# Kernel optimization log

Measured on AMD Instinct MI355X. Metric: run time of the kernel, lower is better.

## Reference

```python
import jax, jax.numpy as jnp
import numpy as np

DECAY_CONSTANT = 1.0


def _build_decay_matrices(weight, decay_value, S, dtype):
    """Build the row-repeat and col-repeat upper-triangular decay matrices.

    Wr[i, j] = w0[i] * (clip(dv0,0.9,1) ** (j-i) / C)   for j >= i, else 0
    Wc[i, j] = w1[j] *  clip(dv1,0.9,1) ** ((j-i) / C)  for j >= i, else 0
    """
    i = jnp.arange(S)[:, None]
    j = jnp.arange(S)[None, :]
    mask = j >= i
    # Clamp exponent to 0 in the masked-out (lower-triangular) region so the
    # power never overflows; values there are discarded by the mask anyway.
    e = jnp.where(mask, (j - i).astype(dtype), jnp.asarray(0.0, dtype))
    dv0 = jnp.clip(decay_value[0, 0], 0.9, 1.0).astype(dtype)
    dv1 = jnp.clip(decay_value[1, 0], 0.9, 1.0).astype(dtype)
    w0 = weight[0].astype(dtype)
    w1 = weight[1].astype(dtype)
    Wr = jnp.where(mask, w0[:, None] * ((dv0 ** e) / DECAY_CONSTANT), jnp.asarray(0.0, dtype))
    Wc = jnp.where(mask, w1[None, :] * (dv1 ** (e / DECAY_CONSTANT)), jnp.asarray(0.0, dtype))
    return Wr, Wc


def setup_inputs() -> dict:
    key = jax.random.key(0)
    kx, kw = jax.random.split(key)
    B, E, S = 4, 2048, 2048
    x = jax.random.normal(kx, (B, E, S), dtype=jnp.float32)
    weight = jax.random.normal(kw, (2, S), dtype=jnp.float32)
    bias = jnp.zeros((S,), dtype=jnp.float32)
    decay_value = jnp.ones((2, 1), dtype=jnp.float32)
    return {"x": x, "weight": weight, "bias": bias, "decay_value": decay_value}


def reference(x, weight, bias, decay_value):
    B, E, S = x.shape
    Wr, Wc = _build_decay_matrices(weight, decay_value, S, x.dtype)
    # x @ Wr + x @ Wc == x @ (Wr + Wc); contract the S axis.
    out = jnp.einsum('bes,st->bet', x, Wr + Wc)  # [B, E, S]
    out = out + bias.astype(x.dtype)
    return out
```

## Files before the change

### kernel.cpp

```cpp
#include <hip/hip_runtime.h>


#define S_LEN 2048
#define EPT 8
#define THREADS 256

__device__ __forceinline__ int sw(int s) { return s ^ ((s >> 3) & 7); }

typedef __attribute__((address_space(1))) const void g1void;
typedef __attribute__((address_space(3))) void l3void;

__global__ __launch_bounds__(THREADS, 8)
void crcl_kernel(const float* __restrict__ x,
                 const float* __restrict__ weight,
                 const float* __restrict__ bias,
                 const float* __restrict__ decay,
                 float* __restrict__ out)
{
    __shared__ float ldsrow[S_LEN];
    __shared__ float carry[2][4];

    const int t    = (int)threadIdx.x;
    const int lane = t & 63;
    const int w    = t >> 6;
    const long row = (long)blockIdx.x;

    const float dv0 = fminf(fmaxf(decay[0], 0.9f), 1.0f);
    const float dv1 = fminf(fmaxf(decay[1], 0.9f), 1.0f);

    float4* lds4 = (float4*)ldsrow;
    const float4* x4 = (const float4*)(x + row * (long)S_LEN);
#pragma unroll
    for (int it = 0; it < 2; ++it) {
        const int s = it * 256 + t;
        __builtin_amdgcn_global_load_lds((g1void*)&x4[sw(s)], (l3void*)&lds4[s],
                                         16, 0, 0);
    }
    __syncthreads();

    const float4* w0_4 = (const float4*)weight;
    float p[EPT], q[EPT];
    float pc = 0.0f, qc = 0.0f;
#pragma unroll
    for (int c = 0; c < 2; ++c) {
        const int s = 2 * t + c;
        const float4 xv = lds4[sw(s)];
        const float4 wv = w0_4[s];
        const float xs[4] = {xv.x, xv.y, xv.z, xv.w};
        const float ws[4] = {wv.x, wv.y, wv.z, wv.w};
#pragma unroll
        for (int j = 0; j < 4; ++j) {
            const int k = 4 * c + j;
            pc = fmaf(dv0, pc, xs[j] * ws[j]);
            qc = fmaf(dv1, qc, xs[j]);
            p[k] = pc;
            q[k] = qc;
        }
    }

    float A8_0 = dv0 * dv0; A8_0 *= A8_0; A8_0 *= A8_0;
    float A8_1 = dv1 * dv1; A8_1 *= A8_1; A8_1 *= A8_1;

    float cp = pc, cq = qc;
    float k0 = A8_0, k1 = A8_1;
#pragma unroll
    for (int d = 1; d < 64; d <<= 1) {
        const float up = __shfl_up(cp, (unsigned)d, 64);
        const float uq = __shfl_up(cq, (unsigned)d, 64);
        if (lane >= d) {
            cp = fmaf(k0, up, cp);
            cq = fmaf(k1, uq, cq);
        }
        k0 *= k0;
        k1 *= k1;
    }
    float cin_p = __shfl_up(cp, 1u, 64);
    float cin_q = __shfl_up(cq, 1u, 64);
    if (lane == 0) { cin_p = 0.0f; cin_q = 0.0f; }

    if (lane == 63) { carry[0][w] = cp; carry[1][w] = cq; }
    __syncthreads();

    float A512_0 = A8_0, A512_1 = A8_1;
#pragma unroll
    for (int b = 0; b < 6; ++b) { A512_0 *= A512_0; A512_1 *= A512_1; }

    float cwp = 0.0f, cwq = 0.0f;
#pragma unroll
    for (int v = 0; v < 3; ++v) {
        if (v < w) {
            cwp = fmaf(cwp, A512_0, carry[0][v]);
            cwq = fmaf(cwq, A512_1, carry[1][v]);
        }
    }
    const float lf = (float)lane;
    const float pw8_0 = exp2f(lf * log2f(A8_0));
    const float pw8_1 = exp2f(lf * log2f(A8_1));
    cin_p = fmaf(cwp, pw8_0, cin_p);
    cin_q = fmaf(cwq, pw8_1, cin_q);

    const float4* w1_4 = (const float4*)(weight + S_LEN);
    const float4* b_4  = (const float4*)bias;
    float pw0 = dv0, pw1 = dv1;
#pragma unroll
    for (int c = 0; c < 2; ++c) {
        const int s = 2 * t + c;
        const float4 wv = w1_4[s];
        const float4 bv = b_4[s];
        float yr[4];
#pragma unroll
        for (int j = 0; j < 4; ++j) {
            const int k = 4 * c + j;
            const float Pk = fmaf(cin_p, pw0, p[k]);
            const float Qk = fmaf(cin_q, pw1, q[k]);
            pw0 *= dv0; pw1 *= dv1;
            const float wj = (j == 0) ? wv.x : (j == 1) ? wv.y : (j == 2) ? wv.z : wv.w;
            const float bj = (j == 0) ? bv.x : (j == 1) ? bv.y : (j == 2) ? bv.z : bv.w;
            yr[j] = fmaf(wj, Qk, Pk) + bj;
        }
        lds4[sw(s)] = make_float4(yr[0], yr[1], yr[2], yr[3]);
    }
    __syncthreads();

    float4* out4 = (float4*)(out + row * (long)S_LEN);
#pragma unroll
    for (int it = 0; it < 2; ++it) {
        const int s = it * 256 + t;
        out4[s] = lds4[sw(s)];
    }
}

extern "C" void kernel_launch(void* const* d_in, const int* in_sizes, int n_in,
                              void* d_out, int out_size, void* d_ws, size_t ws_size,
                              hipStream_t stream) {
    const float* x      = (const float*)d_in[0];
    const float* weight = (const float*)d_in[1];
    const float* bias   = (const float*)d_in[2];
    const float* decay  = (const float*)d_in[3];
    float* out = (float*)d_out;

    const int nrows = in_sizes[0] / S_LEN;
    hipLaunchKernelGGL(crcl_kernel, dim3(nrows), dim3(THREADS), 0, stream,
                       x, weight, bias, decay, out);
}
```

Baseline: 26.65 us.

## Load rows directly into registers and drop LDS staging for input and output

Removes the LDS staging buffer. Each thread now loads its two float4s of x, weights and bias straight from global memory and writes its output with two direct float4 stores, which drops two barriers and the swizzled LDS round trips. The local scan is recomputed in a second pass seeded by the carry-in instead of keeping eight partial values per thread, trading a few extra FMAs for fewer live registers. All loads are issued up front to overlap latency. Direct global accesses at a stride of two float4s per thread are less coalesced than the previous layout.

```diff
diff --git a/kernel.cpp b/kernel.cpp
--- a/kernel.cpp
+++ b/kernel.cpp
@@ -2,13 +2,7 @@
 
 
 #define S_LEN 2048
-#define EPT 8
 #define THREADS 256
-
-__device__ __forceinline__ int sw(int s) { return s ^ ((s >> 3) & 7); }
-
-typedef __attribute__((address_space(1))) const void g1void;
-typedef __attribute__((address_space(3))) void l3void;
 
 __global__ __launch_bounds__(THREADS, 8)
 void crcl_kernel(const float* __restrict__ x,
@@ -17,7 +11,6 @@
                  const float* __restrict__ decay,
                  float* __restrict__ out)
 {
-    __shared__ float ldsrow[S_LEN];
     __shared__ float carry[2][4];
 
     const int t    = (int)threadIdx.x;
@@ -25,37 +18,27 @@
     const int w    = t >> 6;
     const long row = (long)blockIdx.x;
 
+    const float4* x4  = (const float4*)(x + row * (long)S_LEN);
+    const float4* w04 = (const float4*)weight;
+    const float4* w14 = (const float4*)(weight + S_LEN);
+    const float4* b4  = (const float4*)bias;
+
+    const float4 xa = x4[2 * t],  xb = x4[2 * t + 1];
+    const float4 wa = w04[2 * t], wb = w04[2 * t + 1];
+    const float4 va = w14[2 * t], vb = w14[2 * t + 1];
+    const float4 ba = b4[2 * t],  bb = b4[2 * t + 1];
+
     const float dv0 = fminf(fmaxf(decay[0], 0.9f), 1.0f);
     const float dv1 = fminf(fmaxf(decay[1], 0.9f), 1.0f);
 
-    float4* lds4 = (float4*)ldsrow;
-    const float4* x4 = (const float4*)(x + row * (long)S_LEN);
-#pragma unroll
-    for (int it = 0; it < 2; ++it) {
-        const int s = it * 256 + t;
-        __builtin_amdgcn_global_load_lds((g1void*)&x4[sw(s)], (l3void*)&lds4[s],
-                                         16, 0, 0);
-    }
-    __syncthreads();
+    const float xs[8] = {xa.x, xa.y, xa.z, xa.w, xb.x, xb.y, xb.z, xb.w};
+    const float ws[8] = {wa.x, wa.y, wa.z, wa.w, wb.x, wb.y, wb.z, wb.w};
 
-    const float4* w0_4 = (const float4*)weight;
-    float p[EPT], q[EPT];
     float pc = 0.0f, qc = 0.0f;
 #pragma unroll
-    for (int c = 0; c < 2; ++c) {
-        const int s = 2 * t + c;
-        const float4 xv = lds4[sw(s)];
-        const float4 wv = w0_4[s];
-        const float xs[4] = {xv.x, xv.y, xv.z, xv.w};
-        const float ws[4] = {wv.x, wv.y, wv.z, wv.w};
-#pragma unroll
-        for (int j = 0; j < 4; ++j) {
-            const int k = 4 * c + j;
-            pc = fmaf(dv0, pc, xs[j] * ws[j]);
-            qc = fmaf(dv1, qc, xs[j]);
-            p[k] = pc;
-            q[k] = qc;
-        }
+    for (int k = 0; k < 8; ++k) {
+        pc = fmaf(dv0, pc, xs[k] * ws[k]);
+        qc = fmaf(dv1, qc, xs[k]);
     }
 
     float A8_0 = dv0 * dv0; A8_0 *= A8_0; A8_0 *= A8_0;
@@ -93,41 +76,27 @@
             cwq = fmaf(cwq, A512_1, carry[1][v]);
         }
     }
-    const float lf = (float)lane;
-    const float pw8_0 = exp2f(lf * log2f(A8_0));
-    const float pw8_1 = exp2f(lf * log2f(A8_1));
-    cin_p = fmaf(cwp, pw8_0, cin_p);
-    cin_q = fmaf(cwq, pw8_1, cin_q);
+    const float e8 = (float)(8 * lane);
+    const float pwl_0 = exp2f(e8 * log2f(dv0));
+    const float pwl_1 = exp2f(e8 * log2f(dv1));
+    cin_p = fmaf(cwp, pwl_0, cin_p);
+    cin_q = fmaf(cwq, pwl_1, cin_q);
 
-    const float4* w1_4 = (const float4*)(weight + S_LEN);
-    const float4* b_4  = (const float4*)bias;
-    float pw0 = dv0, pw1 = dv1;
+    const float vs[8] = {va.x, va.y, va.z, va.w, vb.x, vb.y, vb.z, vb.w};
+    const float bs[8] = {ba.x, ba.y, ba.z, ba.w, bb.x, bb.y, bb.z, bb.w};
+
+    float p2 = cin_p, q2 = cin_q;
+    float ys[8];
 #pragma unroll
-    for (int c = 0; c < 2; ++c) {
-        const int s = 2 * t + c;
-        const float4 wv = w1_4[s];
-        const float4 bv = b_4[s];
-        float yr[4];
-#pragma unroll
-        for (int j = 0; j < 4; ++j) {
-            const int k = 4 * c + j;
-            const float Pk = fmaf(cin_p, pw0, p[k]);
-            const float Qk = fmaf(cin_q, pw1, q[k]);
-            pw0 *= dv0; pw1 *= dv1;
-            const float wj = (j == 0) ? wv.x : (j == 1) ? wv.y : (j == 2) ? wv.z : wv.w;
-            const float bj = (j == 0) ? bv.x : (j == 1) ? bv.y : (j == 2) ? bv.z : bv.w;
-            yr[j] = fmaf(wj, Qk, Pk) + bj;
-        }
-        lds4[sw(s)] = make_float4(yr[0], yr[1], yr[2], yr[3]);
+    for (int k = 0; k < 8; ++k) {
+        p2 = fmaf(dv0, p2, xs[k] * ws[k]);
+        q2 = fmaf(dv1, q2, xs[k]);
+        ys[k] = fmaf(vs[k], q2, p2) + bs[k];
     }
-    __syncthreads();
 
-    float4* out4 = (float4*)(out + row * (long)S_LEN);
-#pragma unroll
-    for (int it = 0; it < 2; ++it) {
-        const int s = it * 256 + t;
-        out4[s] = lds4[sw(s)];
-    }
+    float4* o4 = (float4*)(out + row * (long)S_LEN);
+    o4[2 * t]     = make_float4(ys[0], ys[1], ys[2], ys[3]);
+    o4[2 * t + 1] = make_float4(ys[4], ys[5], ys[6], ys[7]);
 }
 
 extern "C" void kernel_launch(void* const* d_in, const int* in_sizes, int n_in,
```

Result: no change. 27.13 us (+1.8%).
